# Performance work log

Hardware: AMD Instinct MI355X
Metric: run time of the kernel (lower is better)

## Reference

```python
import jax, jax.numpy as jnp
import numpy as np

N, M, Z_DIM = 32768, 8192, 64


def setup_inputs() -> dict:
    key = jax.random.key(0)
    kz, ke = jax.random.split(key)
    z = jax.random.normal(kz, (N, Z_DIM), dtype=jnp.float32)
    # torch: e = rand(M, z_dim) * 2 - 1  -> uniform in [-1, 1)
    e = jax.random.uniform(ke, (M, Z_DIM), dtype=jnp.float32, minval=-1.0, maxval=1.0)
    return {"z": z, "e": e}


def reference(z, e):
    # data['z'] = tanh(z)
    zt = jnp.tanh(z)                                   # (N, Z)
    # pairwise squared distance via Gram expansion:
    # ||a - b||^2 = ||a||^2 + ||b||^2 - 2 a.b  (same math as the
    # broadcasted sum((a-b)**2) without the (N, M, Z) intermediate)
    zn = jnp.sum(zt * zt, axis=1)                      # (N,)
    en = jnp.sum(e * e, axis=1)                        # (M,)
    distance = zn[:, None] + en[None, :] - 2.0 * (zt @ e.T)   # (N, M)
    # min over the batch dim N for each sample e, then mean over M
    loss = jnp.mean(jnp.min(distance, axis=0))
    return loss
```

## Files before the change

kernel.cpp:

```cpp
#include <hip/hip_runtime.h>
#include <hip/hip_bf16.h>
#include <math.h>

#define NN 32768
#define MM 8192
#define ZD 64
#define WAVES 4
#define MW 64
#define MBLK (WAVES * MW)
#define NMB (MM / MBLK)
#define NCHUNKS 32
#define CHUNK (NN / NCHUNKS)
#define NROWS 128
#define NITER (CHUNK / NROWS)

typedef __attribute__((ext_vector_type(8))) short bf16x8;
typedef __attribute__((ext_vector_type(4))) float f32x4;

__device__ inline unsigned short f2bf(float f) {
  unsigned u = __float_as_uint(f);
  return (unsigned short)((u + 0x7fffu + ((u >> 16) & 1u)) >> 16);
}
__device__ inline float bf2f(unsigned short h) {
  return __uint_as_float(((unsigned)h) << 16);
}

__global__ __launch_bounds__(256) void prep(
    const float* __restrict__ z, const float* __restrict__ e,
    unsigned short* __restrict__ zb, float* __restrict__ zn,
    unsigned short* __restrict__ eb, float* __restrict__ en) {
  const int q = threadIdx.x & 7;
  if (blockIdx.x < NN / 32) {
    const int row = blockIdx.x * 32 + (threadIdx.x >> 3);
    const size_t base = (size_t)row * ZD + q * 8;
    float4 v0 = *reinterpret_cast<const float4*>(&z[base]);
    float4 v1 = *reinterpret_cast<const float4*>(&z[base + 4]);
    float in[8] = {v0.x, v0.y, v0.z, v0.w, v1.x, v1.y, v1.z, v1.w};
    unsigned short b[8];
    float s = 0.f;
#pragma unroll
    for (int i = 0; i < 8; ++i) {
      b[i] = f2bf(tanhf(in[i]));
      float r = bf2f(b[i]);
      s += r * r;
    }
    *reinterpret_cast<bf16x8*>(&zb[base]) = *reinterpret_cast<bf16x8*>(b);
    s += __shfl_xor(s, 1, 64);
    s += __shfl_xor(s, 2, 64);
    s += __shfl_xor(s, 4, 64);
    if (q == 0) zn[row] = s;
  } else {
    const int row = (blockIdx.x - NN / 32) * 32 + (threadIdx.x >> 3);
    const size_t base = (size_t)row * ZD + q * 8;
    float4 v0 = *reinterpret_cast<const float4*>(&e[base]);
    float4 v1 = *reinterpret_cast<const float4*>(&e[base + 4]);
    float in[8] = {v0.x, v0.y, v0.z, v0.w, v1.x, v1.y, v1.z, v1.w};
    unsigned short b[8];
    float s = 0.f;
#pragma unroll
    for (int i = 0; i < 8; ++i) {
      unsigned short qb = f2bf(in[i]);
      float r = bf2f(qb);
      s += r * r;
      b[i] = f2bf(-2.f * r);
    }
    *reinterpret_cast<bf16x8*>(&eb[base]) = *reinterpret_cast<bf16x8*>(b);
    s += __shfl_xor(s, 1, 64);
    s += __shfl_xor(s, 2, 64);
    s += __shfl_xor(s, 4, 64);
    if (q == 0) en[row] = s;
  }
}

__global__ __launch_bounds__(256, 4) void min_dist(
    const unsigned short* __restrict__ zb, const unsigned short* __restrict__ eb,
    const float* __restrict__ zn, float* __restrict__ partial) {
  __shared__ __align__(128) unsigned short zlds[2][NROWS * ZD];
  const int wg = ((blockIdx.x & 7) << 7) + (blockIdx.x >> 3);
  const int mb = wg & (NMB - 1);
  const int cb = wg >> 5;
  const int lane = threadIdx.x & 63;
  const int wv = threadIdx.x >> 6;
  const int lr = lane & 15;
  const int lg = lane >> 4;
  const int m0 = mb * MBLK + wv * MW;
  const int nb0 = cb * CHUNK;

  const int srow = lane >> 3;
  const int sslot = (lane & 7) ^ srow;
  const char* zsrc = (const char*)zb + (size_t)nb0 * 128 +
                     (wv * 32 + srow) * 128 + (sslot << 4);
  char* ldst0 = (char*)&zlds[0][0] + wv * 4096;
  char* ldst1 = (char*)&zlds[1][0] + wv * 4096;

  bf16x8 bfr[4][2];
#pragma unroll
  for (int t = 0; t < 4; ++t)
#pragma unroll
    for (int h = 0; h < 2; ++h)
      bfr[t][h] = *reinterpret_cast<const bf16x8*>(
          &eb[(size_t)(m0 + t * 16 + lr) * ZD + h * 32 + lg * 8]);

  float minv[4] = {3.4e38f, 3.4e38f, 3.4e38f, 3.4e38f};

  auto stage = [&](char* dst, const char* src) {
#pragma unroll
    for (int j = 0; j < 4; ++j)
      __builtin_amdgcn_global_load_lds(
          (const __attribute__((address_space(1))) unsigned int*)(src + j * 1024),
          (__attribute__((address_space(3))) unsigned int*)(dst + j * 1024),
          16, 0, 0);
  };

  const float* znp = zn + nb0;
  const int x0 = (lg * 16) ^ ((lr & 7) << 4);

  stage(ldst0, zsrc);
  zsrc += NROWS * 128;
  __syncthreads();

  for (int it = 0; it < NITER; ++it) {
    const char* lbase = (it & 1) ? (const char*)&zlds[1][0] : (const char*)&zlds[0][0];
    if (it + 1 < NITER) {
      stage((it & 1) ? ldst0 : ldst1, zsrc);
      zsrc += NROWS * 128;
    }
#pragma unroll
    for (int s = 0; s < NROWS / 16; ++s) {
      const int rb = (s * 16 + lr) * 128;
      bf16x8 a0 = *reinterpret_cast<const bf16x8*>(lbase + rb + x0);
      bf16x8 a1 = *reinterpret_cast<const bf16x8*>(lbase + rb + (x0 ^ 64));
      f32x4 znv = *reinterpret_cast<const f32x4*>(znp + s * 16 + lg * 4);
#pragma unroll
      for (int t = 0; t < 4; ++t) {
        f32x4 acc = __builtin_amdgcn_mfma_f32_16x16x32_bf16(a0, bfr[t][0], znv, 0, 0, 0);
        acc = __builtin_amdgcn_mfma_f32_16x16x32_bf16(a1, bfr[t][1], acc, 0, 0, 0);
        float x = fminf(fminf(acc[0], acc[1]), acc[2]);
        minv[t] = fminf(fminf(x, acc[3]), minv[t]);
      }
    }
    znp += NROWS;
    __syncthreads();
  }

#pragma unroll
  for (int t = 0; t < 4; ++t) {
    float v = minv[t];
    v = fminf(v, __shfl_xor(v, 16, 64));
    v = fminf(v, __shfl_xor(v, 32, 64));
    if (lg == 0) partial[(size_t)cb * MM + m0 + t * 16 + lr] = v;
  }
}

__global__ __launch_bounds__(256) void finalize1(const float* __restrict__ partial,
                                                 const float* __restrict__ en,
                                                 double* __restrict__ bsum) {
  const int m = blockIdx.x * 256 + threadIdx.x;
  float mv = partial[m];
#pragma unroll
  for (int c = 1; c < NCHUNKS; ++c)
    mv = fminf(mv, partial[(size_t)c * MM + m]);
  double s = (double)(mv + en[m]);
  __shared__ double sred[256];
  sred[threadIdx.x] = s;
  __syncthreads();
  for (int off = 128; off > 0; off >>= 1) {
    if ((int)threadIdx.x < off) sred[threadIdx.x] += sred[threadIdx.x + off];
    __syncthreads();
  }
  if (threadIdx.x == 0) bsum[blockIdx.x] = sred[0];
}

__global__ __launch_bounds__(64) void finalize2(const double* __restrict__ bsum,
                                                float* __restrict__ out) {
  double s = (threadIdx.x < MM / 256) ? bsum[threadIdx.x] : 0.0;
  s += __shfl_xor(s, 1, 64);
  s += __shfl_xor(s, 2, 64);
  s += __shfl_xor(s, 4, 64);
  s += __shfl_xor(s, 8, 64);
  s += __shfl_xor(s, 16, 64);
  s += __shfl_xor(s, 32, 64);
  if (threadIdx.x == 0) out[0] = (float)(s / (double)MM);
}

extern "C" void kernel_launch(void* const* d_in, const int* in_sizes, int n_in,
                              void* d_out, int out_size, void* d_ws, size_t ws_size,
                              hipStream_t stream) {
  const float* z = (const float*)d_in[0];
  const float* e = (const float*)d_in[1];
  float* out = (float*)d_out;

  unsigned short* zb = (unsigned short*)d_ws;
  unsigned short* eb = zb + (size_t)NN * ZD;
  float* zn = (float*)(eb + (size_t)MM * ZD);
  float* en = zn + NN;
  float* partial = en + MM;
  double* bsum = (double*)(partial + (size_t)NCHUNKS * MM);

  prep<<<(NN + MM) / 32, 256, 0, stream>>>(z, e, zb, zn, eb, en);
  min_dist<<<NMB * NCHUNKS, 256, 0, stream>>>(zb, eb, zn, partial);
  finalize1<<<MM / 256, 256, 0, stream>>>(partial, en, bsum);
  finalize2<<<1, 64, 0, stream>>>(bsum, out);
}
```

Before: 46.90 us.

## Switch to 32x32 MFMA, atomic min for partials, and fuse finalize kernels

```diff
diff --git a/kernel.cpp b/kernel.cpp
--- a/kernel.cpp
+++ b/kernel.cpp
@@ -13,9 +13,11 @@
 #define CHUNK (NN / NCHUNKS)
 #define NROWS 128
 #define NITER (CHUNK / NROWS)
+#define SCALE 4294967296.0
 
 typedef __attribute__((ext_vector_type(8))) short bf16x8;
 typedef __attribute__((ext_vector_type(4))) float f32x4;
+typedef __attribute__((ext_vector_type(16))) float f32x16;
 
 __device__ inline unsigned short f2bf(float f) {
   unsigned u = __float_as_uint(f);
@@ -28,7 +30,9 @@
 __global__ __launch_bounds__(256) void prep(
     const float* __restrict__ z, const float* __restrict__ e,
     unsigned short* __restrict__ zb, float* __restrict__ zn,
-    unsigned short* __restrict__ eb, float* __restrict__ en) {
+    unsigned short* __restrict__ eb, float* __restrict__ en,
+    unsigned* __restrict__ dmin, unsigned long long* __restrict__ acc,
+    unsigned* __restrict__ cnt) {
   const int q = threadIdx.x & 7;
   if (blockIdx.x < NN / 32) {
     const int row = blockIdx.x * 32 + (threadIdx.x >> 3);
@@ -68,21 +72,28 @@
     s += __shfl_xor(s, 1, 64);
     s += __shfl_xor(s, 2, 64);
     s += __shfl_xor(s, 4, 64);
-    if (q == 0) en[row] = s;
+    if (q == 0) {
+      en[row] = s;
+      dmin[row] = 0xFFFFFFFFu;
+    }
+    if (blockIdx.x == NN / 32 && threadIdx.x == 0) {
+      *acc = 0ULL;
+      *cnt = 0u;
+    }
   }
 }
 
 __global__ __launch_bounds__(256, 4) void min_dist(
     const unsigned short* __restrict__ zb, const unsigned short* __restrict__ eb,
-    const float* __restrict__ zn, float* __restrict__ partial) {
+    const float* __restrict__ zn, unsigned* __restrict__ dmin) {
   __shared__ __align__(128) unsigned short zlds[2][NROWS * ZD];
   const int wg = ((blockIdx.x & 7) << 7) + (blockIdx.x >> 3);
   const int mb = wg & (NMB - 1);
   const int cb = wg >> 5;
   const int lane = threadIdx.x & 63;
   const int wv = threadIdx.x >> 6;
-  const int lr = lane & 15;
-  const int lg = lane >> 4;
+  const int lc = lane & 31;
+  const int hi = lane >> 5;
   const int m0 = mb * MBLK + wv * MW;
   const int nb0 = cb * CHUNK;
 
@@ -93,15 +104,15 @@
   char* ldst0 = (char*)&zlds[0][0] + wv * 4096;
   char* ldst1 = (char*)&zlds[1][0] + wv * 4096;
 
-  bf16x8 bfr[4][2];
-#pragma unroll
-  for (int t = 0; t < 4; ++t)
-#pragma unroll
-    for (int h = 0; h < 2; ++h)
-      bfr[t][h] = *reinterpret_cast<const bf16x8*>(
-          &eb[(size_t)(m0 + t * 16 + lr) * ZD + h * 32 + lg * 8]);
-
-  float minv[4] = {3.4e38f, 3.4e38f, 3.4e38f, 3.4e38f};
+  bf16x8 bfr[2][4];
+#pragma unroll
+  for (int t = 0; t < 2; ++t)
+#pragma unroll
+    for (int kk = 0; kk < 4; ++kk)
+      bfr[t][kk] = *reinterpret_cast<const bf16x8*>(
+          &eb[(size_t)(m0 + t * 32 + lc) * ZD + kk * 16 + hi * 8]);
+
+  float minv[2] = {3.4e38f, 3.4e38f};
 
   auto stage = [&](char* dst, const char* src) {
 #pragma unroll
@@ -113,7 +124,6 @@
   };
 
   const float* znp = zn + nb0;
-  const int x0 = (lg * 16) ^ ((lr & 7) << 4);
 
   stage(ldst0, zsrc);
   zsrc += NROWS * 128;
@@ -126,17 +136,36 @@
       zsrc += NROWS * 128;
     }
 #pragma unroll
-    for (int s = 0; s < NROWS / 16; ++s) {
-      const int rb = (s * 16 + lr) * 128;
-      bf16x8 a0 = *reinterpret_cast<const bf16x8*>(lbase + rb + x0);
-      bf16x8 a1 = *reinterpret_cast<const bf16x8*>(lbase + rb + (x0 ^ 64));
-      f32x4 znv = *reinterpret_cast<const f32x4*>(znp + s * 16 + lg * 4);
-#pragma unroll
-      for (int t = 0; t < 4; ++t) {
-        f32x4 acc = __builtin_amdgcn_mfma_f32_16x16x32_bf16(a0, bfr[t][0], znv, 0, 0, 0);
-        acc = __builtin_amdgcn_mfma_f32_16x16x32_bf16(a1, bfr[t][1], acc, 0, 0, 0);
-        float x = fminf(fminf(acc[0], acc[1]), acc[2]);
-        minv[t] = fminf(fminf(x, acc[3]), minv[t]);
+    for (int s = 0; s < NROWS / 32; ++s) {
+      const int rb = (s * 32 + lc) * 128;
+      bf16x8 a[4];
+#pragma unroll
+      for (int kk = 0; kk < 4; ++kk)
+        a[kk] = *reinterpret_cast<const bf16x8*>(
+            lbase + rb + ((((kk << 1) + hi) ^ (lane & 7)) << 4));
+      f32x16 znc;
+#pragma unroll
+      for (int g = 0; g < 4; ++g) {
+        f32x4 L = *reinterpret_cast<const f32x4*>(znp + s * 32 + g * 8 + hi * 4);
+        znc[g * 4 + 0] = L[0];
+        znc[g * 4 + 1] = L[1];
+        znc[g * 4 + 2] = L[2];
+        znc[g * 4 + 3] = L[3];
+      }
+#pragma unroll
+      for (int t = 0; t < 2; ++t) {
+        f32x16 accv = znc;
+#pragma unroll
+        for (int kk = 0; kk < 4; ++kk)
+          accv = __builtin_amdgcn_mfma_f32_32x32x16_bf16(a[kk], bfr[t][kk], accv, 0, 0, 0);
+        float x0 = fminf(fminf(accv[0], accv[1]), accv[2]);
+        float x1 = fminf(fminf(accv[3], accv[4]), accv[5]);
+        float x2 = fminf(fminf(accv[6], accv[7]), accv[8]);
+        float x3 = fminf(fminf(accv[9], accv[10]), accv[11]);
+        float x4 = fminf(fminf(accv[12], accv[13]), accv[14]);
+        float y0 = fminf(fminf(x0, x1), x2);
+        float y1 = fminf(fminf(x3, x4), accv[15]);
+        minv[t] = fminf(fminf(y0, y1), minv[t]);
       }
     }
     znp += NROWS;
@@ -144,22 +173,26 @@
   }
 
 #pragma unroll
-  for (int t = 0; t < 4; ++t) {
+  for (int t = 0; t < 2; ++t) {
     float v = minv[t];
-    v = fminf(v, __shfl_xor(v, 16, 64));
     v = fminf(v, __shfl_xor(v, 32, 64));
-    if (lg == 0) partial[(size_t)cb * MM + m0 + t * 16 + lr] = v;
-  }
-}
-
-__global__ __launch_bounds__(256) void finalize1(const float* __restrict__ partial,
-                                                 const float* __restrict__ en,
-                                                 double* __restrict__ bsum) {
+    if (lane < 32) {
+      unsigned bits = __float_as_uint(v);
+      unsigned key = (bits & 0x80000000u) ? ~bits : (bits | 0x80000000u);
+      atomicMin(&dmin[m0 + t * 32 + lane], key);
+    }
+  }
+}
+
+__global__ __launch_bounds__(256) void finalize(const unsigned* __restrict__ dmin,
+                                                const float* __restrict__ en,
+                                                unsigned long long* __restrict__ acc,
+                                                unsigned* __restrict__ cnt,
+                                                float* __restrict__ out) {
   const int m = blockIdx.x * 256 + threadIdx.x;
-  float mv = partial[m];
-#pragma unroll
-  for (int c = 1; c < NCHUNKS; ++c)
-    mv = fminf(mv, partial[(size_t)c * MM + m]);
+  unsigned key = dmin[m];
+  unsigned bits = (key & 0x80000000u) ? (key & 0x7FFFFFFFu) : ~key;
+  float mv = __uint_as_float(bits);
   double s = (double)(mv + en[m]);
   __shared__ double sred[256];
   sred[threadIdx.x] = s;
@@ -168,19 +201,17 @@
     if ((int)threadIdx.x < off) sred[threadIdx.x] += sred[threadIdx.x + off];
     __syncthreads();
   }
-  if (threadIdx.x == 0) bsum[blockIdx.x] = sred[0];
-}
-
-__global__ __launch_bounds__(64) void finalize2(const double* __restrict__ bsum,
-                                                float* __restrict__ out) {
-  double s = (threadIdx.x < MM / 256) ? bsum[threadIdx.x] : 0.0;
-  s += __shfl_xor(s, 1, 64);
-  s += __shfl_xor(s, 2, 64);
-  s += __shfl_xor(s, 4, 64);
-  s += __shfl_xor(s, 8, 64);
-  s += __shfl_xor(s, 16, 64);
-  s += __shfl_xor(s, 32, 64);
-  if (threadIdx.x == 0) out[0] = (float)(s / (double)MM);
+  if (threadIdx.x == 0) {
+    unsigned long long iv = (unsigned long long)(sred[0] * SCALE + 0.5);
+    atomicAdd(acc, iv);
+    __threadfence();
+    unsigned d = atomicAdd(cnt, 1u);
+    if (d == MM / 256 - 1) {
+      __threadfence();
+      unsigned long long tot = atomicAdd(acc, 0ULL);
+      out[0] = (float)((double)tot / SCALE / (double)MM);
+    }
+  }
 }
 
 extern "C" void kernel_launch(void* const* d_in, const int* in_sizes, int n_in,
@@ -194,11 +225,11 @@
   unsigned short* eb = zb + (size_t)NN * ZD;
   float* zn = (float*)(eb + (size_t)MM * ZD);
   float* en = zn + NN;
-  float* partial = en + MM;
-  double* bsum = (double*)(partial + (size_t)NCHUNKS * MM);
-
-  prep<<<(NN + MM) / 32, 256, 0, stream>>>(z, e, zb, zn, eb, en);
-  min_dist<<<NMB * NCHUNKS, 256, 0, stream>>>(zb, eb, zn, partial);
-  finalize1<<<MM / 256, 256, 0, stream>>>(partial, en, bsum);
-  finalize2<<<1, 64, 0, stream>>>(bsum, out);
-}
+  unsigned* dmin = (unsigned*)(en + MM);
+  unsigned long long* acc = (unsigned long long*)(dmin + MM);
+  unsigned* cnt = (unsigned*)(acc + 1);
+
+  prep<<<(NN + MM) / 32, 256, 0, stream>>>(z, e, zb, zn, eb, en, dmin, acc, cnt);
+  min_dist<<<NMB * NCHUNKS, 256, 0, stream>>>(zb, eb, zn, dmin);
+  finalize<<<MM / 256, 256, 0, stream>>>(dmin, en, acc, cnt, out);
+}
```

New measurement: 51.14 us. 9.0% more time.
